# Kernel optimization log

Measured on AMD Instinct MI355X. Metric: run time of the kernel, lower is better.

The kernel has to match this reference:

```python
import jax, jax.numpy as jnp
import numpy as np

B, L, D = 8, 4096, 512
KS = (3, 5, 7)
EPS = 1e-5
W_SCALE = 0.02  # tame torch.randn-style init for numerical sanity


def layernorm(x, g, b):
    mu = jnp.mean(x, axis=-1, keepdims=True)
    var = jnp.var(x, axis=-1, keepdims=True)
    return (x - mu) * jax.lax.rsqrt(var + EPS) * g + b


def masked_conv(x1, chain, W, b):
    # x1: (B, C, L); W: (O, C, K); chain: (B, L) int32
    K = W.shape[2]
    pad_l = (K - 1) // 2
    pad_r = (K - 1) - pad_l
    xp = jnp.pad(x1, ((0, 0), (0, 0), (pad_l, pad_r)))
    ip = jnp.pad(chain, ((0, 0), (pad_l, pad_r)))  # pad id = 0
    Lx = x1.shape[2]
    # center tap of each window is the position's own chain id (odd K, center == pad_l)
    out = b[None, :, None]
    for k in range(K):  # small static loop over taps
        xs = xp[:, :, k:k + Lx]                      # (B, C, L)
        mk = (ip[:, k:k + Lx] == chain)              # (B, L) bool
        out = out + jnp.einsum('bcl,oc->bol', xs * mk[:, None, :], W[:, :, k])
    return out


def setup_inputs() -> dict:
    key = jax.random.key(0)
    ks = jax.random.split(key, 16)
    inp = {
        'x': jax.random.normal(ks[0], (B, L, D), dtype=jnp.float32),
        'chain': jnp.sort(jax.random.randint(ks[1], (B, L), 0, 8), axis=-1).astype(jnp.int32),
    }
    for i, (name, K) in enumerate(zip(('W3', 'W5', 'W7'), KS)):
        inp[name] = jax.random.normal(ks[2 + i], (D, D, K), dtype=jnp.float32) * W_SCALE
        inp['b' + name[1:]] = jax.random.normal(ks[5 + i], (D,), dtype=jnp.float32) * W_SCALE
    inp['mlp_w1'] = jax.random.normal(ks[8], (D, 4 * D), dtype=jnp.float32) * W_SCALE
    inp['mlp_b1'] = jnp.zeros((4 * D,), dtype=jnp.float32)
    inp['mlp_w2'] = jax.random.normal(ks[9], (4 * D, D), dtype=jnp.float32) * W_SCALE
    inp['mlp_b2'] = jnp.zeros((D,), dtype=jnp.float32)
    inp['ln1_g'] = jnp.ones((D,), dtype=jnp.float32)
    inp['ln1_b'] = jnp.zeros((D,), dtype=jnp.float32)
    inp['ln2_g'] = jnp.ones((D,), dtype=jnp.float32)
    inp['ln2_b'] = jnp.zeros((D,), dtype=jnp.float32)
    return inp


def reference(x, chain, W3, b3, W5, b5, W7, b7,
              mlp_w1, mlp_b1, mlp_w2, mlp_b2,
              ln1_g, ln1_b, ln2_g, ln2_b):
    x1 = jnp.transpose(x, (0, 2, 1))  # (B, C, L)
    for W, b in ((W3, b3), (W5, b5), (W7, b7)):
        x1 = masked_conv(x1, chain, W, b)
    h = layernorm(x + jnp.transpose(x1, (0, 2, 1)), ln1_g, ln1_b)
    mlp = jax.nn.gelu(h @ mlp_w1 + mlp_b1) @ mlp_w2 + mlp_b2
    return layernorm(h + mlp, ln2_g, ln2_b)
```

## Files before the change

### kernel.cpp

```cpp
#include <hip/hip_runtime.h>
#include <math.h>

#define BB 8
#define LL 4096
#define DD 512
#define PTOT (BB*LL)
#define HID  2048

typedef __attribute__((ext_vector_type(8))) short short8;
typedef __attribute__((ext_vector_type(4))) float f32x4;

typedef __attribute__((address_space(1))) const unsigned int gconst_u32;
typedef __attribute__((address_space(3))) unsigned int lds_u32;

__device__ __forceinline__ void gload16(const void* g, void* l) {
    __builtin_amdgcn_global_load_lds((gconst_u32*)g, (lds_u32*)l, 16, 0, 0);
}

__device__ __forceinline__ unsigned short f2bf(float f) {
    union { float f; unsigned int u; } v; v.f = f;
    unsigned int r = v.u + 0x7fffu + ((v.u >> 16) & 1u);
    return (unsigned short)(r >> 16);
}
__device__ __forceinline__ float bf2f(unsigned short h) {
    union { unsigned int u; float f; } v; v.u = ((unsigned int)h) << 16;
    return v.f;
}
__device__ __forceinline__ float gelu_fast(float x) {
    float x2 = x * x;
    float t  = x * fmaf(0.044715f, x2, 1.0f);
    float e  = __builtin_amdgcn_exp2f(-2.3021143f * t);
    return x * __builtin_amdgcn_rcpf(1.0f + e);
}

__device__ __forceinline__ void barrier_sync() {
    asm volatile("" ::: "memory");
    __builtin_amdgcn_s_barrier();
    asm volatile("" ::: "memory");
}
#define WAITV(N) asm volatile("s_waitcnt vmcnt(" #N ")" ::: "memory")
#define WAITL0() asm volatile("s_waitcnt lgkmcnt(0)" ::: "memory")
#define SCHED0() __builtin_amdgcn_sched_barrier(0)

__global__ __launch_bounds__(256) void convert_x(const float* __restrict__ x,
                                                 unsigned short* __restrict__ xb,
                                                 unsigned short* __restrict__ zp) {
    int tid = blockIdx.x * 256 + threadIdx.x;
    if (blockIdx.x == 0 && threadIdx.x < 128) zp[threadIdx.x] = 0;
    float4 v = ((const float4*)x)[tid];
    uint2 o;
    o.x = (unsigned int)f2bf(v.x) | ((unsigned int)f2bf(v.y) << 16);
    o.y = (unsigned int)f2bf(v.z) | ((unsigned int)f2bf(v.w) << 16);
    ((uint2*)xb)[tid] = o;
}

__global__ __launch_bounds__(256) void trans_wconv(const float* __restrict__ W,
                                                   unsigned short* __restrict__ Wt, int K) {
    int tid = blockIdx.x * 256 + threadIdx.x;
    if (tid >= DD * DD * K) return;
    int o  = tid / (K * DD);
    int kc = tid - o * K * DD;
    int k  = kc >> 9;
    int c  = kc & (DD - 1);
    Wt[tid] = f2bf(W[(o * DD + c) * K + k]);
}

__global__ __launch_bounds__(256) void trans_w1(const float* __restrict__ W,
                                                unsigned short* __restrict__ Wt) {
    int tid = blockIdx.x * 256 + threadIdx.x;
    int n = tid >> 9;
    int c = tid & (DD - 1);
    Wt[tid] = f2bf(W[c * HID + n]);
}

__global__ __launch_bounds__(256) void trans_w2(const float* __restrict__ W,
                                                unsigned short* __restrict__ Wt) {
    int tid = blockIdx.x * 256 + threadIdx.x;
    int n = tid >> 11;
    int h = tid & (HID - 1);
    Wt[tid] = f2bf(W[h * DD + n]);
}

__global__ __launch_bounds__(256) void make_srcp(const int* __restrict__ chain,
                                                 int* __restrict__ srcp, int K) {
    int tid = blockIdx.x * 256 + threadIdx.x;
    if (tid >= PTOT * K) return;
    int p = tid / K;
    int k = tid - p * K;
    int b = p >> 12;
    int l = p & (LL - 1);
    int pad = (K - 1) >> 1;
    int l2 = l + k - pad;
    bool ok = (l2 >= 0) && (l2 < LL) && (chain[b * LL + l2] == chain[b * LL + l]);
    srcp[tid] = ok ? (p + k - pad) : -1;
}

template <int TAPS, int EPI>
__global__ __launch_bounds__(512) void mfma_gemm4(
        const unsigned short* __restrict__ A, int lda,
        const int* __restrict__ srcp,
        const unsigned short* __restrict__ Bt, int ldb,
        const float* __restrict__ bias,
        void* __restrict__ Yv, int ldc, int Kspan,
        const unsigned short* __restrict__ zp) {
    __shared__ alignas(16) unsigned short As[2 * 256 * 64];
    __shared__ alignas(16) unsigned short Bs[2 * 256 * 64];
    __shared__ int srcp_s[TAPS > 0 ? 256 * TAPS : 4];

    const int t = threadIdx.x;
    const int lane = t & 63, w = t >> 6;
    const int wr = w & 1, wc = w >> 1;
    const int lm = lane & 15, qh = lane >> 4, x7 = lane & 7;
    const int qq = (lane & 7) ^ (lane >> 3);
    const int l3 = lane >> 3;
    const int p0 = blockIdx.x * 256;
    const int o0 = blockIdx.y * 256;
    const int NKT = TAPS ? TAPS * 8 : (Kspan >> 6);

    f32x4 acc[8][4];
#pragma unroll
    for (int mi = 0; mi < 8; mi++)
#pragma unroll
        for (int nj = 0; nj < 4; nj++) acc[mi][nj] = (f32x4){0.f, 0.f, 0.f, 0.f};

    auto stgB = [&](int h) {
        if (h >= 4 * NKT) return;
        int jt = h >> 2;
        int rb = (h & 2) ? 128 : 0;
        unsigned short* dst = Bs + (jt & 1) * 16384 + (rb + w * 16) * 64;
        int kb = jt << 6;
#pragma unroll
        for (int i = 0; i < 2; i++) {
            int rl = rb + w * 16 + i * 8 + l3;
            gload16(Bt + (size_t)(o0 + rl) * ldb + kb + qq * 8, dst + i * 512);
        }
    };
    auto stgA = [&](int h, int sp0, int sp1) {
        if (h >= 4 * NKT) return;
        int jt = h >> 2;
        int rb = (h & 2) ? 128 : 0;
        unsigned short* dst = As + (jt & 1) * 16384 + (rb + w * 16) * 64;
#pragma unroll
        for (int i = 0; i < 2; i++) {
            const unsigned short* g;
            if (TAPS) {
                int sp = i ? sp1 : sp0;
                g = (sp >= 0) ? (A + (size_t)sp * lda + (jt & 7) * 64 + qq * 8) : zp;
            } else {
                int rl = rb + w * 16 + i * 8 + l3;
                g = A + (size_t)(p0 + rl) * lda + (jt << 6) + qq * 8;
            }
            gload16(g, dst + i * 512);
        }
    };
    auto ldsp = [&](int h, int& sp0, int& sp1) {
        if (TAPS && h < 4 * NKT) {
            int jt = h >> 2, tap = jt >> 3;
            int rb = (h & 2) ? 128 : 0;
            int rl = rb + w * 16 + l3;
            sp0 = srcp_s[rl * TAPS + tap];
            sp1 = srcp_s[(rl + 8) * TAPS + tap];
        }
    };

    if (TAPS) {
        for (int idx = t; idx < 256 * TAPS; idx += 512)
            srcp_s[idx] = srcp[(size_t)p0 * TAPS + idx];
    }
    __syncthreads();
    int sp0 = -1, sp1 = -1;
    ldsp(0, sp0, sp1); stgA(0, sp0, sp1);
    stgB(1);
    ldsp(2, sp0, sp1); stgA(2, sp0, sp1);
    stgB(3);
    ldsp(4, sp0, sp1); stgA(4, sp0, sp1);
    stgB(5);
    ldsp(6, sp0, sp1);
    WAITV(4);
    barrier_sync();

#define RD_A(MIH) do {                                                          \
    _Pragma("unroll")                                                           \
    for (int kk = 0; kk < 2; kk++) {                                            \
        int sa = ((kk * 4 + qh) ^ x7) * 8;                                      \
        _Pragma("unroll")                                                       \
        for (int m = 0; m < 4; m++)                                             \
            af[m][kk] = *(const short8*)&as_[((((MIH)*4+m)*2 + wr)*16 + lm)*64 + sa]; \
    } } while (0)
#define RD_B(NJH, BF) do {                                                      \
    _Pragma("unroll")                                                           \
    for (int kk = 0; kk < 2; kk++) {                                            \
        int sa = ((kk * 4 + qh) ^ x7) * 8;                                      \
        _Pragma("unroll")                                                       \
        for (int n = 0; n < 2; n++)                                             \
            BF[n][kk] = *(const short8*)&bs_[((((NJH)*2+n)*4 + wc)*16 + lm)*64 + sa]; \
    } } while (0)
#define MFMA_Q(MIH, NJH, BF)                                                    \
    __builtin_amdgcn_s_setprio(1);                                              \
    _Pragma("unroll")                                                           \
    for (int kk = 0; kk < 2; kk++)                                              \
        _Pragma("unroll")                                                       \
        for (int m = 0; m < 4; m++)                                             \
            _Pragma("unroll")                                                   \
            for (int n = 0; n < 2; n++)                                         \
                acc[(MIH)*4+m][(NJH)*2+n] = __builtin_amdgcn_mfma_f32_16x16x32_bf16( \
                    af[m][kk], BF[n][kk], acc[(MIH)*4+m][(NJH)*2+n], 0, 0, 0);  \
    __builtin_amdgcn_s_setprio(0);                                              \
    SCHED0()

    short8 af[4][2], bf0[2][2], bf1[2][2];
#pragma unroll 1
    for (int kt = 0; kt < NKT; ++kt) {
        const unsigned short* as_ = As + (kt & 1) * 16384;
        const unsigned short* bs_ = Bs + (kt & 1) * 16384;
        const bool last = (kt == NKT - 1);
        RD_A(0); RD_B(0, bf0);
        if (!last) stgA(4 * kt + 6, sp0, sp1);
        WAITL0(); SCHED0();
        MFMA_Q(0, 0, bf0);
        if (!last) ldsp(4 * kt + 8, sp0, sp1);
        barrier_sync();
        RD_B(1, bf1);
        if (!last) stgB(4 * kt + 7);
        WAITL0(); SCHED0();
        MFMA_Q(0, 1, bf1);
        barrier_sync();
        RD_A(1);
        if (!last) stgA(4 * kt + 8, sp0, sp1);
        WAITL0(); SCHED0();
        MFMA_Q(1, 0, bf0);
        if (!last) ldsp(4 * kt + 10, sp0, sp1);
        barrier_sync();
        if (!last) stgB(4 * kt + 9);
        WAITL0(); SCHED0();
        MFMA_Q(1, 1, bf1);
        if (kt == NKT - 2) { WAITV(0); } else if (!last) { WAITV(4); }
        barrier_sync();
    }
#undef RD_A
#undef RD_B
#undef MFMA_Q

#pragma unroll
    for (int mi = 0; mi < 8; mi++) {
#pragma unroll
        for (int nj = 0; nj < 4; nj++) {
            int col = o0 + (nj * 4 + wc) * 16 + lm;
#pragma unroll
            for (int r = 0; r < 4; r++) {
                int row = p0 + (mi * 2 + wr) * 16 + qh * 4 + r;
                float v = acc[mi][nj][r];
                size_t idx = (size_t)row * ldc + col;
                if (EPI == 0) {
                    ((unsigned short*)Yv)[idx] = f2bf(v + bias[col]);
                } else if (EPI == 1) {
                    ((unsigned short*)Yv)[idx] = f2bf(gelu_fast(v + bias[col]));
                } else if (EPI == 2) {
                    ((float*)Yv)[idx] = v + bias[col];
                } else {
                    ((float*)Yv)[idx] += v;
                }
            }
        }
    }
}

__global__ __launch_bounds__(256) void ln1_kernel(const float* __restrict__ x,
                                                  const unsigned short* __restrict__ conv,
                                                  const float* __restrict__ g,
                                                  const float* __restrict__ beta,
                                                  unsigned short* __restrict__ h) {
    int p = blockIdx.x, t = threadIdx.x;
    size_t base = (size_t)p * DD;
    float v0 = x[base + t] + bf2f(conv[base + t]);
    float v1 = x[base + 256 + t] + bf2f(conv[base + 256 + t]);
    float s = v0 + v1, sq = v0 * v0 + v1 * v1;
#pragma unroll
    for (int off = 32; off > 0; off >>= 1) { s += __shfl_xor(s, off); sq += __shfl_xor(sq, off); }
    __shared__ float red[2][4];
    int wid = t >> 6, lane = t & 63;
    if (lane == 0) { red[0][wid] = s; red[1][wid] = sq; }
    __syncthreads();
    float S = red[0][0] + red[0][1] + red[0][2] + red[0][3];
    float SQ = red[1][0] + red[1][1] + red[1][2] + red[1][3];
    float mu = S * (1.f / DD);
    float var = SQ * (1.f / DD) - mu * mu;
    float rs = rsqrtf(var + 1e-5f);
    h[base + t]       = f2bf((v0 - mu) * rs * g[t] + beta[t]);
    h[base + 256 + t] = f2bf((v1 - mu) * rs * g[256 + t] + beta[256 + t]);
}

__global__ __launch_bounds__(256) void ln2_kernel(const unsigned short* __restrict__ h,
                                                  float* __restrict__ out,
                                                  const float* __restrict__ g,
                                                  const float* __restrict__ beta) {
    int p = blockIdx.x, t = threadIdx.x;
    size_t base = (size_t)p * DD;
    float v0 = bf2f(h[base + t]) + out[base + t];
    float v1 = bf2f(h[base + 256 + t]) + out[base + 256 + t];
    float s = v0 + v1, sq = v0 * v0 + v1 * v1;
#pragma unroll
    for (int off = 32; off > 0; off >>= 1) { s += __shfl_xor(s, off); sq += __shfl_xor(sq, off); }
    __shared__ float red[2][4];
    int wid = t >> 6, lane = t & 63;
    if (lane == 0) { red[0][wid] = s; red[1][wid] = sq; }
    __syncthreads();
    float S = red[0][0] + red[0][1] + red[0][2] + red[0][3];
    float SQ = red[1][0] + red[1][1] + red[1][2] + red[1][3];
    float mu = S * (1.f / DD);
    float var = SQ * (1.f / DD) - mu * mu;
    float rs = rsqrtf(var + 1e-5f);
    out[base + t]       = (v0 - mu) * rs * g[t] + beta[t];
    out[base + 256 + t] = (v1 - mu) * rs * g[256 + t] + beta[256 + t];
}

extern "C" void kernel_launch(void* const* d_in, const int* in_sizes, int n_in,
                              void* d_out, int out_size, void* d_ws, size_t ws_size,
                              hipStream_t stream) {
    const float* x     = (const float*)d_in[0];
    const int*   chain = (const int*)d_in[1];
    const float* W3    = (const float*)d_in[2];
    const float* b3    = (const float*)d_in[3];
    const float* W5    = (const float*)d_in[4];
    const float* b5    = (const float*)d_in[5];
    const float* W7    = (const float*)d_in[6];
    const float* b7    = (const float*)d_in[7];
    const float* w1    = (const float*)d_in[8];
    const float* bm1   = (const float*)d_in[9];
    const float* w2    = (const float*)d_in[10];
    const float* bm2   = (const float*)d_in[11];
    const float* g1    = (const float*)d_in[12];
    const float* be1   = (const float*)d_in[13];
    const float* g2    = (const float*)d_in[14];
    const float* be2   = (const float*)d_in[15];
    float* out = (float*)d_out;

    const size_t ACT = (size_t)PTOT * DD * 2;
    char* ws = (char*)d_ws;
    size_t off = 0;
    unsigned short* Xb   = (unsigned short*)(ws + off); off += ACT;
    unsigned short* buf1 = (unsigned short*)(ws + off); off += ACT;
    unsigned short* buf2 = (unsigned short*)(ws + off); off += ACT;
    unsigned short* w3t  = (unsigned short*)(ws + off); off += (size_t)3 * DD * DD * 2;
    unsigned short* w5t  = (unsigned short*)(ws + off); off += (size_t)5 * DD * DD * 2;
    unsigned short* w7t  = (unsigned short*)(ws + off); off += (size_t)7 * DD * DD * 2;
    unsigned short* w1t  = (unsigned short*)(ws + off); off += (size_t)DD * HID * 2;
    unsigned short* w2t  = (unsigned short*)(ws + off); off += (size_t)DD * HID * 2;
    int* srcp3 = (int*)(ws + off); off += (size_t)PTOT * 3 * 4;
    int* srcp5 = (int*)(ws + off); off += (size_t)PTOT * 5 * 4;
    int* srcp7 = (int*)(ws + off); off += (size_t)PTOT * 7 * 4;
    unsigned short* zp = (unsigned short*)(ws + off); off += 256;
    size_t base_off = off;
    bool full = (ws_size >= base_off + (size_t)PTOT * HID * 2);
    unsigned short* Hb = (unsigned short*)(ws + base_off);

    convert_x<<<PTOT * DD / (256 * 4), 256, 0, stream>>>(x, Xb, zp);
    trans_wconv<<<(DD * DD * 3 + 255) / 256, 256, 0, stream>>>(W3, w3t, 3);
    trans_wconv<<<(DD * DD * 5 + 255) / 256, 256, 0, stream>>>(W5, w5t, 5);
    trans_wconv<<<(DD * DD * 7 + 255) / 256, 256, 0, stream>>>(W7, w7t, 7);
    trans_w1<<<DD * HID / 256, 256, 0, stream>>>(w1, w1t);
    trans_w2<<<DD * HID / 256, 256, 0, stream>>>(w2, w2t);
    make_srcp<<<(PTOT * 3 + 255) / 256, 256, 0, stream>>>(chain, srcp3, 3);
    make_srcp<<<(PTOT * 5 + 255) / 256, 256, 0, stream>>>(chain, srcp5, 5);
    make_srcp<<<(PTOT * 7 + 255) / 256, 256, 0, stream>>>(chain, srcp7, 7);

    dim3 gconv(PTOT / 256, DD / 256);

    mfma_gemm4<3, 0><<<gconv, 512, 0, stream>>>(Xb, DD, srcp3, w3t, 3 * DD, b3, buf1, DD, DD, zp);
    mfma_gemm4<5, 0><<<gconv, 512, 0, stream>>>(buf1, DD, srcp5, w5t, 5 * DD, b5, buf2, DD, DD, zp);
    mfma_gemm4<7, 0><<<gconv, 512, 0, stream>>>(buf2, DD, srcp7, w7t, 7 * DD, b7, buf1, DD, DD, zp);

    ln1_kernel<<<PTOT, 256, 0, stream>>>(x, buf1, g1, be1, buf2);

    if (full) {
        dim3 g1d(PTOT / 256, HID / 256);
        mfma_gemm4<0, 1><<<g1d, 512, 0, stream>>>(buf2, DD, nullptr, w1t, DD, bm1,
                                                  Hb, HID, DD, zp);
        mfma_gemm4<0, 2><<<gconv, 512, 0, stream>>>(Hb, HID, nullptr, w2t, HID, bm2,
                                                    out, DD, HID, zp);
    } else {
        for (int jc = 0; jc < 4; jc++) {
            mfma_gemm4<0, 1><<<gconv, 512, 0, stream>>>(buf2, DD, nullptr,
                                                        w1t + (size_t)jc * DD * DD, DD,
                                                        bm1 + jc * DD, Hb, DD, DD, zp);
            if (jc == 0)
                mfma_gemm4<0, 2><<<gconv, 512, 0, stream>>>(Hb, DD, nullptr,
                                                            w2t + jc * DD, HID, bm2,
                                                            out, DD, DD, zp);
            else
                mfma_gemm4<0, 3><<<gconv, 512, 0, stream>>>(Hb, DD, nullptr,
                                                            w2t + jc * DD, HID, bm2,
                                                            out, DD, DD, zp);
        }
    }

    ln2_kernel<<<PTOT, 256, 0, stream>>>(buf2, out, g2, be2);
}
```

Baseline: 668.2 us.

## Merge GEMM k-loop phases from four barriers to two per iteration

Restructures the main MFMA loop so both B fragments are read from LDS up front and two MFMA quarters run back-to-back, with the A and B global-to-LDS stages issued together. This halves the barrier count per k-tile and removes the scheduler hint after each MFMA group, aiming to cut synchronization stalls. In exchange it holds more fragment registers live at once and issues prefetch loads in larger bursts, which may raise register pressure or reduce load/compute interleaving.

```diff
diff --git a/kernel.cpp b/kernel.cpp
--- a/kernel.cpp
+++ b/kernel.cpp
@@ -96,7 +96,7 @@
 }
 
 template <int TAPS, int EPI>
-__global__ __launch_bounds__(512) void mfma_gemm4(
+__global__ __launch_bounds__(512) void mfma_gemm6(
         const unsigned short* __restrict__ A, int lda,
         const int* __restrict__ srcp,
         const unsigned short* __restrict__ Bt, int ldb,
@@ -205,8 +205,7 @@
             for (int n = 0; n < 2; n++)                                         \
                 acc[(MIH)*4+m][(NJH)*2+n] = __builtin_amdgcn_mfma_f32_16x16x32_bf16( \
                     af[m][kk], BF[n][kk], acc[(MIH)*4+m][(NJH)*2+n], 0, 0, 0);  \
-    __builtin_amdgcn_s_setprio(0);                                              \
-    SCHED0()
+    __builtin_amdgcn_s_setprio(0)
 
     short8 af[4][2], bf0[2][2], bf1[2][2];
 #pragma unroll 1
@@ -214,26 +213,19 @@
         const unsigned short* as_ = As + (kt & 1) * 16384;
         const unsigned short* bs_ = Bs + (kt & 1) * 16384;
         const bool last = (kt == NKT - 1);
-        RD_A(0); RD_B(0, bf0);
-        if (!last) stgA(4 * kt + 6, sp0, sp1);
+        RD_A(0); RD_B(0, bf0); RD_B(1, bf1);
+        if (!last) { stgA(4 * kt + 6, sp0, sp1); stgB(4 * kt + 7); }
         WAITL0(); SCHED0();
         MFMA_Q(0, 0, bf0);
+        MFMA_Q(0, 1, bf1);
         if (!last) ldsp(4 * kt + 8, sp0, sp1);
         barrier_sync();
-        RD_B(1, bf1);
-        if (!last) stgB(4 * kt + 7);
-        WAITL0(); SCHED0();
-        MFMA_Q(0, 1, bf1);
-        barrier_sync();
         RD_A(1);
-        if (!last) stgA(4 * kt + 8, sp0, sp1);
+        if (!last) { stgA(4 * kt + 8, sp0, sp1); stgB(4 * kt + 9); }
         WAITL0(); SCHED0();
         MFMA_Q(1, 0, bf0);
+        MFMA_Q(1, 1, bf1);
         if (!last) ldsp(4 * kt + 10, sp0, sp1);
-        barrier_sync();
-        if (!last) stgB(4 * kt + 9);
-        WAITL0(); SCHED0();
-        MFMA_Q(1, 1, bf1);
         if (kt == NKT - 2) { WAITV(0); } else if (!last) { WAITV(4); }
         barrier_sync();
     }
@@ -366,29 +358,29 @@
 
     dim3 gconv(PTOT / 256, DD / 256);
 
-    mfma_gemm4<3, 0><<<gconv, 512, 0, stream>>>(Xb, DD, srcp3, w3t, 3 * DD, b3, buf1, DD, DD, zp);
-    mfma_gemm4<5, 0><<<gconv, 512, 0, stream>>>(buf1, DD, srcp5, w5t, 5 * DD, b5, buf2, DD, DD, zp);
-    mfma_gemm4<7, 0><<<gconv, 512, 0, stream>>>(buf2, DD, srcp7, w7t, 7 * DD, b7, buf1, DD, DD, zp);
+    mfma_gemm6<3, 0><<<gconv, 512, 0, stream>>>(Xb, DD, srcp3, w3t, 3 * DD, b3, buf1, DD, DD, zp);
+    mfma_gemm6<5, 0><<<gconv, 512, 0, stream>>>(buf1, DD, srcp5, w5t, 5 * DD, b5, buf2, DD, DD, zp);
+    mfma_gemm6<7, 0><<<gconv, 512, 0, stream>>>(buf2, DD, srcp7, w7t, 7 * DD, b7, buf1, DD, DD, zp);
 
     ln1_kernel<<<PTOT, 256, 0, stream>>>(x, buf1, g1, be1, buf2);
 
     if (full) {
         dim3 g1d(PTOT / 256, HID / 256);
-        mfma_gemm4<0, 1><<<g1d, 512, 0, stream>>>(buf2, DD, nullptr, w1t, DD, bm1,
+        mfma_gemm6<0, 1><<<g1d, 512, 0, stream>>>(buf2, DD, nullptr, w1t, DD, bm1,
                                                   Hb, HID, DD, zp);
-        mfma_gemm4<0, 2><<<gconv, 512, 0, stream>>>(Hb, HID, nullptr, w2t, HID, bm2,
+        mfma_gemm6<0, 2><<<gconv, 512, 0, stream>>>(Hb, HID, nullptr, w2t, HID, bm2,
                                                     out, DD, HID, zp);
     } else {
         for (int jc = 0; jc < 4; jc++) {
-            mfma_gemm4<0, 1><<<gconv, 512, 0, stream>>>(buf2, DD, nullptr,
+            mfma_gemm6<0, 1><<<gconv, 512, 0, stream>>>(buf2, DD, nullptr,
                                                         w1t + (size_t)jc * DD * DD, DD,
                                                         bm1 + jc * DD, Hb, DD, DD, zp);
             if (jc == 0)
-                mfma_gemm4<0, 2><<<gconv, 512, 0, stream>>>(Hb, DD, nullptr,
+                mfma_gemm6<0, 2><<<gconv, 512, 0, stream>>>(Hb, DD, nullptr,
                                                             w2t + jc * DD, HID, bm2,
                                                             out, DD, DD, zp);
             else
-                mfma_gemm4<0, 3><<<gconv, 512, 0, stream>>>(Hb, DD, nullptr,
+                mfma_gemm6<0, 3><<<gconv, 512, 0, stream>>>(Hb, DD, nullptr,
                                                             w2t + jc * DD, HID, bm2,
                                                             out, DD, DD, zp);
         }
```

Result: faster. 652.7 us (-2.3%).
